# Kernel tuning notes

Hardware: AMD Instinct MI355X
Metric: run time of the kernel (lower is better)

## Reference

```python
import jax, jax.numpy as jnp
import numpy as np

N_NODES = 50000
N_EDGES = 800000
F_IN, H1, H2, N_CLASSES = 128, 200, 100, 40


def setup_inputs() -> dict:
    key = jax.random.key(0)
    ks = jax.random.split(key, 8)
    x = jax.random.normal(ks[0], (N_NODES, F_IN), dtype=jnp.float32)
    edge_index = jax.random.randint(ks[1], (2, N_EDGES), 0, N_NODES, dtype=jnp.int64)
    # Glorot-ish scaled params
    W1 = jax.random.normal(ks[2], (F_IN, H1), dtype=jnp.float32) * (1.0 / np.sqrt(F_IN))
    b1 = jnp.zeros((H1,), dtype=jnp.float32)
    W2 = jax.random.normal(ks[3], (H1, H2), dtype=jnp.float32) * (1.0 / np.sqrt(H1))
    b2 = jnp.zeros((H2,), dtype=jnp.float32)
    Wout = jax.random.normal(ks[4], (H2, N_CLASSES), dtype=jnp.float32) * (1.0 / np.sqrt(H2))
    bout = jnp.zeros((N_CLASSES,), dtype=jnp.float32)
    return {"x": x, "edge_index": edge_index, "W1": W1, "b1": b1,
            "W2": W2, "b2": b2, "Wout": Wout, "bout": bout}


def _gcn_norm(edge_index, n_nodes):
    # Add self-loops, then symmetric normalization deg^{-1/2}[src]*deg^{-1/2}[dst]
    loop = jnp.arange(n_nodes, dtype=edge_index.dtype)
    src = jnp.concatenate([edge_index[0], loop])
    dst = jnp.concatenate([edge_index[1], loop])
    deg = jax.ops.segment_sum(jnp.ones_like(dst, dtype=jnp.float32), dst,
                              num_segments=n_nodes)
    dinv = jax.lax.rsqrt(deg)  # deg >= 1 due to self-loops
    norm = dinv[src] * dinv[dst]  # [E+N]
    return src, dst, norm


def _gcn_conv(h, W, b, src, dst, norm, n_nodes):
    hw = h @ W                                   # [N, out] dense transform first
    msg = norm[:, None] * hw[src]                # [E+N, out] gather + scale
    agg = jax.ops.segment_sum(msg, dst, num_segments=n_nodes)  # scatter-add
    return agg + b


def reference(x, edge_index, W1, b1, W2, b2, Wout, bout):
    n = x.shape[0]
    src, dst, norm = _gcn_norm(edge_index, n)
    h = jax.nn.relu(_gcn_conv(x, W1, b1, src, dst, norm, n))
    # dropout is identity in eval mode
    h = jax.nn.relu(_gcn_conv(h, W2, b2, src, dst, norm, n))
    return h @ Wout + bout
```

## Files before the change

### kernel.cpp

```cpp
#include <hip/hip_runtime.h>


#define NN 50000
#define NE 800000
#define NPART 8
#define PCAP 20
#define DST 40

typedef short v8s __attribute__((ext_vector_type(8)));
typedef float f4 __attribute__((ext_vector_type(4)));
typedef ushort u8v __attribute__((ext_vector_type(8)));

static __device__ __forceinline__ ushort bf16rne(float f) {
    unsigned u = __float_as_uint(f);
    return (ushort)((u + 0x7FFFu + ((u >> 16) & 1u)) >> 16);
}
static __device__ __forceinline__ float bf16tof(ushort h) {
    return __uint_as_float(((unsigned)h) << 16);
}

#define PK1 (14 * 4 * 512)
#define PK2 (7 * 7 * 512)
#define PK3 (3 * 4 * 512)
#define ZERO_BLKS ((NN * NPART / 4 + 255) / 256)
#define PACK_BLKS ((PK1 + PK2 + PK3 + 255) / 256)

__global__ __launch_bounds__(256)
void prep_kernel(const float* __restrict__ W1, const float* __restrict__ W2,
                 const float* __restrict__ W3,
                 ushort* __restrict__ b1p, ushort* __restrict__ b2p,
                 ushort* __restrict__ b3p,
                 int* __restrict__ flag, int* __restrict__ cnt8,
                 const unsigned int* __restrict__ eiw) {
    int b = blockIdx.x;
    if (b < ZERO_BLKS) {
        int i = b * 256 + threadIdx.x;
        if (i < NN * NPART / 4) ((int4*)cnt8)[i] = make_int4(0, 0, 0, 0);
        return;
    }
    b -= ZERO_BLKS;
    if (b < PACK_BLKS) {
        int idx = b * 256 + threadIdx.x;
        const float* W; ushort* o; int q, KS, K, N;
        if (idx < PK1)                  { W = W1; o = b1p; q = idx;             KS = 4; K = 128; N = 200; }
        else if (idx < PK1 + PK2)       { W = W2; o = b2p; q = idx - PK1;       KS = 7; K = 200; N = 100; }
        else if (idx < PK1 + PK2 + PK3) { W = W3; o = b3p; q = idx - PK1 - PK2; KS = 4; K = 100; N = 40;  }
        else return;
        int tile = q / (KS * 512);
        int rem  = q % (KS * 512);
        int s    = rem / 512;
        int z    = rem % 512;
        int lane = z / 8, j = z % 8;
        int col = tile * 16 + (lane & 15);
        int k   = s * 32 + (lane >> 4) * 8 + j;
        o[q] = bf16rne((k < K && col < N) ? W[k * N + col] : 0.f);
        return;
    }
    if (threadIdx.x == 0) {
        int is64 = 1;
        for (int i = 0; i < 32; ++i)
            if (eiw[2 * i + 1] != 0u) { is64 = 0; break; }
        *flag = is64;
    }
}

__global__ __launch_bounds__(256)
void place8_kernel(const void* __restrict__ ei, const int* __restrict__ flag,
                   int* __restrict__ cnt8, ushort* __restrict__ slab) {
    int e = blockIdx.x * 256 + threadIdx.x;
    if (e >= NE) return;
    int p = blockIdx.x & 7;
    int s, d;
    if (*flag) {
        s = (int)((const long long*)ei)[e];
        d = (int)((const long long*)ei)[NE + e];
    } else {
        s = ((const int*)ei)[e];
        d = ((const int*)ei)[NE + e];
    }
    int pos = atomicAdd(&cnt8[p * NN + d], 1);
    if (pos < PCAP) slab[((size_t)p * NN + d) * PCAP + pos] = (ushort)s;
}

__global__ __launch_bounds__(256)
void build_kernel(const int* __restrict__ cnt8, const ushort* __restrict__ slab,
                  const float* __restrict__ x, ushort* __restrict__ csrF,
                  int* __restrict__ degC, float* __restrict__ dinv,
                  ushort* __restrict__ xb) {
    __shared__ float sdinv[256];
    const int t = threadIdx.x;
    const int d = blockIdx.x * 256 + t;
    if (d < NN) {
        int tot = 0, k = 0;
        ushort* __restrict__ dst = csrF + (size_t)d * DST;
        #pragma unroll
        for (int p = 0; p < NPART; ++p) {
            int c = cnt8[p * NN + d];
            tot += c;
            c = min(c, PCAP);
            const ushort* sp = slab + ((size_t)p * NN + d) * PCAP;
            for (int j = 0; j < c; ++j) {
                if (k < DST) dst[k++] = sp[j];
            }
        }
        degC[d] = k;
        float di = rsqrtf((float)(tot + 1));
        dinv[d] = di;
        sdinv[t] = di;
    }
    __syncthreads();
    const size_t base = (size_t)blockIdx.x * 256;
    #pragma unroll
    for (int it = 0; it < 16; ++it) {
        int v = it * 256 + t;
        int lrow = v >> 4;
        if (base + lrow >= NN) break;
        float di = sdinv[lrow];
        size_t g = (base + lrow) * 128 + (size_t)(v & 15) * 8;
        float4 v0 = *(const float4*)(x + g);
        float4 v1 = *(const float4*)(x + g + 4);
        *(ushort4*)(xb + g) = make_ushort4(bf16rne(di * v0.x), bf16rne(di * v0.y),
                                           bf16rne(di * v0.z), bf16rne(di * v0.w));
        *(ushort4*)(xb + g + 4) = make_ushort4(bf16rne(di * v1.x), bf16rne(di * v1.y),
                                               bf16rne(di * v1.z), bf16rne(di * v1.w));
    }
}

template <int F, int SST, int KPAD, bool BR>
__global__ __launch_bounds__(256)
void agg_kernel(const ushort* __restrict__ src, const float* __restrict__ dinv,
                const int* __restrict__ degC, const ushort* __restrict__ csrF,
                const float* __restrict__ bias, ushort* __restrict__ outp) {
    const int w = threadIdx.x >> 6, l = threadIdx.x & 63;
    const int grp = l >> 4, cp = l & 15;
    const int row = blockIdx.x * 16 + w * 4 + grp;
    const int cb = cp * 8;
    const int len = degC[row];
    const int s0 = row * DST;
    const float di = dinv[row];
    int lmax = len;
    lmax = max(lmax, __shfl_xor(lmax, 16));
    lmax = max(lmax, __shfl_xor(lmax, 32));

    float acc[8];
    u8v sv = *(const u8v*)(src + (size_t)row * SST + cb);
    #pragma unroll
    for (int q = 0; q < 8; ++q) acc[q] = bf16tof(sv[q]);

    for (int er = 0; er < lmax; er += 8) {
        int c[8];
        float m[8];
        #pragma unroll
        for (int i = 0; i < 8; ++i) {
            bool ok = (er + i) < len;
            c[i] = csrF[ok ? (s0 + er + i) : 0];
            m[i] = ok ? 1.f : 0.f;
        }
        u8v r[8];
        #pragma unroll
        for (int i = 0; i < 8; ++i)
            r[i] = *(const u8v*)(src + (size_t)c[i] * SST + cb);
        #pragma unroll
        for (int i = 0; i < 8; ++i)
            #pragma unroll
            for (int q = 0; q < 8; ++q)
                acc[q] = fmaf(bf16tof(r[i][q]), m[i], acc[q]);
    }

    u8v ov;
    #pragma unroll
    for (int q = 0; q < 8; ++q) {
        int col = cb + q;
        float v = di * acc[q];
        if constexpr (BR) v = (col < F) ? fmaxf(v + bias[col], 0.f) : 0.f;
        else              v = (col < F) ? v : 0.f;
        ov[q] = bf16rne(v);
    }
    *(u8v*)(outp + (size_t)row * KPAD + cb) = ov;
}

template <int NT, int KS, int MODE>
__global__ __launch_bounds__(256)
void mfma_gemm(const ushort* __restrict__ A, const ushort* __restrict__ B,
               float* __restrict__ Cf, ushort* __restrict__ Cb,
               const float* __restrict__ bias, const float* __restrict__ dinv,
               int M, int N, int NPAD) {
    constexpr int KP = KS * 32;
    const int tid = threadIdx.x, w = tid >> 6, l = tid & 63;
    const int arow = blockIdx.x * 64 + w * 16 + (l & 15);
    const int kg = l >> 4;
    const bool aok = arow < M;
    f4 acc[NT];
    #pragma unroll
    for (int t = 0; t < NT; ++t) acc[t] = (f4)0.f;
    const v8s zz = (v8s)0;
    const ushort* pa = A + (size_t)arow * KP + kg * 8;

    for (int s = 0; s < KS; ++s) {
        v8s a = aok ? *(const v8s*)(pa + s * 32) : zz;
        #pragma unroll
        for (int t = 0; t < NT; ++t) {
            v8s b = *(const v8s*)(B + ((size_t)(t * KS + s) * 64 + l) * 8);
            acc[t] = __builtin_amdgcn_mfma_f32_16x16x32_bf16(a, b, acc[t], 0, 0, 0);
        }
    }
    const int crow0 = blockIdx.x * 64 + w * 16 + (l >> 4) * 4;
    #pragma unroll
    for (int t = 0; t < NT; ++t) {
        int col = t * 16 + (l & 15);
        #pragma unroll
        for (int r = 0; r < 4; ++r) {
            int row = crow0 + r;
            if (row >= M) continue;
            float v = acc[t][r];
            if constexpr (MODE == 0) {
                if (col < N) Cf[(size_t)row * N + col] = v + bias[col];
            } else if constexpr (MODE == 1) {
                float o = (col < N) ? fmaxf(v + bias[col], 0.f) : 0.f;
                Cb[(size_t)row * NPAD + col] = bf16rne(o);
            } else {
                float o = (col < N) ? dinv[row] * v : 0.f;
                Cb[(size_t)row * NPAD + col] = bf16rne(o);
            }
        }
    }
}

extern "C" void kernel_launch(void* const* d_in, const int* in_sizes, int n_in,
                              void* d_out, int out_size, void* d_ws, size_t ws_size,
                              hipStream_t stream) {
    const float* x    = (const float*)d_in[0];
    const void*  ei   = d_in[1];
    const float* W1   = (const float*)d_in[2];
    const float* b1   = (const float*)d_in[3];
    const float* W2   = (const float*)d_in[4];
    const float* b2   = (const float*)d_in[5];
    const float* Wout = (const float*)d_in[6];
    const float* bout = (const float*)d_in[7];
    float* out = (float*)d_out;

    char* ws = (char*)d_ws;
    size_t off = 0;
    auto alloc = [&](size_t bytes) -> void* {
        off = (off + 255) & ~(size_t)255;
        void* p = ws + off;
        off += bytes;
        return p;
    };
    int*    flag = (int*)alloc(4);
    int*    cnt8 = (int*)alloc((size_t)NN * NPART * 4);
    int*    degC = (int*)alloc((size_t)NN * 4);
    float*  dinv = (float*)alloc((size_t)NN * 4);
    ushort* slab = (ushort*)alloc((size_t)NN * NPART * PCAP * 2);
    ushort* csrF = (ushort*)alloc((size_t)NN * DST * 2);
    ushort* xb   = (ushort*)alloc((size_t)NN * 128 * 2);
    ushort* tbuf = (ushort*)alloc((size_t)NN * 128 * 2);
    ushort* h1   = (ushort*)alloc((size_t)NN * 224 * 2);
    ushort* u    = (ushort*)alloc((size_t)NN * 128 * 2);
    ushort* h2   = (ushort*)alloc((size_t)NN * 128 * 2);
    ushort* b1p  = (ushort*)alloc((size_t)PK1 * 2);
    ushort* b2p  = (ushort*)alloc((size_t)PK2 * 2);
    ushort* b3p  = (ushort*)alloc((size_t)PK3 * 2);
    (void)ws_size; (void)in_sizes; (void)n_in; (void)out_size;

    const int PREP_BLKS = ZERO_BLKS + PACK_BLKS + 1;

    prep_kernel<<<PREP_BLKS, 256, 0, stream>>>(W1, W2, Wout, b1p, b2p, b3p,
                                               flag, cnt8, (const unsigned int*)ei);
    place8_kernel<<<(NE + 255) / 256, 256, 0, stream>>>(ei, flag, cnt8, slab);
    build_kernel<<<(NN + 255) / 256, 256, 0, stream>>>(cnt8, slab, x, csrF,
                                                       degC, dinv, xb);

    const int GA = NN / 16;
    const int GG = (NN + 63) / 64;

    agg_kernel<128, 128, 128, false><<<GA, 256, 0, stream>>>(
        xb, dinv, degC, csrF, nullptr, tbuf);
    mfma_gemm<14, 4, 1><<<GG, 256, 0, stream>>>(
        tbuf, b1p, nullptr, h1, b1, nullptr, NN, 200, 224);
    mfma_gemm<7, 7, 2><<<GG, 256, 0, stream>>>(
        h1, b2p, nullptr, u, nullptr, dinv, NN, 100, 128);
    agg_kernel<100, 128, 128, true><<<GA, 256, 0, stream>>>(
        u, dinv, degC, csrF, b2, h2);
    mfma_gemm<3, 4, 0><<<GG, 256, 0, stream>>>(
        h2, b3p, out, nullptr, bout, nullptr, NN, 40, 0);
}
```

Baseline: 191.7 us.

## Fuse layer-1 and layer-2 GEMMs via LDS, fuse final GEMM into aggregation

Merges the two dense transforms (128->200 and 200->100) into one kernel that keeps the 200-wide hidden activations in LDS instead of writing and reading them from global memory. It also fuses the output projection (100->40) into the second aggregation kernel, which runs the small MFMA on the 16 aggregated rows held in LDS. This cuts two kernel launches and removes the global round trips for h1 and h2. The cost is more LDS use and fewer concurrent blocks in the fused GEMM, and a partially idle final MFMA stage where one of the four waves does nothing.

Measured after the change: 165.5 us. -13.7%, faster.

```diff
diff --git a/kernel.cpp b/kernel.cpp
--- a/kernel.cpp
+++ b/kernel.cpp
@@ -126,11 +126,10 @@
     }
 }
 
-template <int F, int SST, int KPAD, bool BR>
-__global__ __launch_bounds__(256)
-void agg_kernel(const ushort* __restrict__ src, const float* __restrict__ dinv,
-                const int* __restrict__ degC, const ushort* __restrict__ csrF,
-                const float* __restrict__ bias, ushort* __restrict__ outp) {
+__global__ __launch_bounds__(256)
+void agg1_kernel(const ushort* __restrict__ src, const float* __restrict__ dinv,
+                 const int* __restrict__ degC, const ushort* __restrict__ csrF,
+                 ushort* __restrict__ outp) {
     const int w = threadIdx.x >> 6, l = threadIdx.x & 63;
     const int grp = l >> 4, cp = l & 15;
     const int row = blockIdx.x * 16 + w * 4 + grp;
@@ -143,7 +142,7 @@
     lmax = max(lmax, __shfl_xor(lmax, 32));
 
     float acc[8];
-    u8v sv = *(const u8v*)(src + (size_t)row * SST + cb);
+    u8v sv = *(const u8v*)(src + (size_t)row * 128 + cb);
     #pragma unroll
     for (int q = 0; q < 8; ++q) acc[q] = bf16tof(sv[q]);
 
@@ -159,7 +158,7 @@
         u8v r[8];
         #pragma unroll
         for (int i = 0; i < 8; ++i)
-            r[i] = *(const u8v*)(src + (size_t)c[i] * SST + cb);
+            r[i] = *(const u8v*)(src + (size_t)c[i] * 128 + cb);
         #pragma unroll
         for (int i = 0; i < 8; ++i)
             #pragma unroll
@@ -169,59 +168,141 @@
 
     u8v ov;
     #pragma unroll
+    for (int q = 0; q < 8; ++q) ov[q] = bf16rne(di * acc[q]);
+    *(u8v*)(outp + (size_t)row * 128 + cb) = ov;
+}
+
+__global__ __launch_bounds__(256)
+void gemm12_kernel(const ushort* __restrict__ A, const ushort* __restrict__ B1,
+                   const ushort* __restrict__ B2, const float* __restrict__ b1,
+                   const float* __restrict__ dinv, ushort* __restrict__ u) {
+    constexpr int LST = 232;
+    __shared__ ushort lh1[64 * LST];
+    const int tid = threadIdx.x, w = tid >> 6, l = tid & 63;
+    const int kg = l >> 4;
+    const int arow = blockIdx.x * 64 + w * 16 + (l & 15);
+    const bool aok = arow < NN;
+    const v8s zz = (v8s)0;
+
+    f4 o1[14];
+    #pragma unroll
+    for (int t = 0; t < 14; ++t) o1[t] = (f4)0.f;
+    const ushort* pa = A + (size_t)arow * 128 + kg * 8;
+    for (int s = 0; s < 4; ++s) {
+        v8s a = aok ? *(const v8s*)(pa + s * 32) : zz;
+        #pragma unroll
+        for (int t = 0; t < 14; ++t) {
+            v8s b = *(const v8s*)(B1 + ((size_t)(t * 4 + s) * 64 + l) * 8);
+            o1[t] = __builtin_amdgcn_mfma_f32_16x16x32_bf16(a, b, o1[t], 0, 0, 0);
+        }
+    }
+    const int lrow0 = w * 16 + ((l >> 4) << 2);
+    #pragma unroll
+    for (int t = 0; t < 14; ++t) {
+        int col = t * 16 + (l & 15);
+        float bc = (col < 200) ? b1[col] : 0.f;
+        #pragma unroll
+        for (int r = 0; r < 4; ++r) {
+            float v = (col < 200) ? fmaxf(o1[t][r] + bc, 0.f) : 0.f;
+            lh1[(lrow0 + r) * LST + col] = bf16rne(v);
+        }
+    }
+    __syncthreads();
+    f4 o2[7];
+    #pragma unroll
+    for (int t = 0; t < 7; ++t) o2[t] = (f4)0.f;
+    const int lrowA = w * 16 + (l & 15);
+    for (int s = 0; s < 7; ++s) {
+        v8s a = *(const v8s*)(&lh1[lrowA * LST + kg * 8 + s * 32]);
+        #pragma unroll
+        for (int t = 0; t < 7; ++t) {
+            v8s b = *(const v8s*)(B2 + ((size_t)(t * 7 + s) * 64 + l) * 8);
+            o2[t] = __builtin_amdgcn_mfma_f32_16x16x32_bf16(a, b, o2[t], 0, 0, 0);
+        }
+    }
+    const int crow0 = blockIdx.x * 64 + w * 16 + ((l >> 4) << 2);
+    #pragma unroll
+    for (int t = 0; t < 7; ++t) {
+        int col = t * 16 + (l & 15);
+        #pragma unroll
+        for (int r = 0; r < 4; ++r) {
+            int row = crow0 + r;
+            if (row >= NN) continue;
+            float o = (col < 100) ? dinv[row] * o2[t][r] : 0.f;
+            u[(size_t)row * 128 + col] = bf16rne(o);
+        }
+    }
+}
+
+__global__ __launch_bounds__(256)
+void agg2g3_kernel(const ushort* __restrict__ u, const float* __restrict__ dinv,
+                   const int* __restrict__ degC, const ushort* __restrict__ csrF,
+                   const ushort* __restrict__ B3, const float* __restrict__ b2,
+                   const float* __restrict__ bout, float* __restrict__ out) {
+    constexpr int LST = 136;
+    __shared__ ushort lh2[16 * LST];
+    const int w = threadIdx.x >> 6, l = threadIdx.x & 63;
+    const int grp = l >> 4, cp = l & 15;
+    const int row = blockIdx.x * 16 + w * 4 + grp;
+    const int cb = cp * 8;
+    const int len = degC[row];
+    const int s0 = row * DST;
+    const float di = dinv[row];
+    int lmax = len;
+    lmax = max(lmax, __shfl_xor(lmax, 16));
+    lmax = max(lmax, __shfl_xor(lmax, 32));
+
+    float acc[8];
+    u8v sv = *(const u8v*)(u + (size_t)row * 128 + cb);
+    #pragma unroll
+    for (int q = 0; q < 8; ++q) acc[q] = bf16tof(sv[q]);
+
+    for (int er = 0; er < lmax; er += 8) {
+        int c[8];
+        float m[8];
+        #pragma unroll
+        for (int i = 0; i < 8; ++i) {
+            bool ok = (er + i) < len;
+            c[i] = csrF[ok ? (s0 + er + i) : 0];
+            m[i] = ok ? 1.f : 0.f;
+        }
+        u8v r[8];
+        #pragma unroll
+        for (int i = 0; i < 8; ++i)
+            r[i] = *(const u8v*)(u + (size_t)c[i] * 128 + cb);
+        #pragma unroll
+        for (int i = 0; i < 8; ++i)
+            #pragma unroll
+            for (int q = 0; q < 8; ++q)
+                acc[q] = fmaf(bf16tof(r[i][q]), m[i], acc[q]);
+    }
+    u8v ov;
+    #pragma unroll
     for (int q = 0; q < 8; ++q) {
         int col = cb + q;
         float v = di * acc[q];
-        if constexpr (BR) v = (col < F) ? fmaxf(v + bias[col], 0.f) : 0.f;
-        else              v = (col < F) ? v : 0.f;
+        v = (col < 100) ? fmaxf(v + b2[col], 0.f) : 0.f;
         ov[q] = bf16rne(v);
     }
-    *(u8v*)(outp + (size_t)row * KPAD + cb) = ov;
-}
-
-template <int NT, int KS, int MODE>
-__global__ __launch_bounds__(256)
-void mfma_gemm(const ushort* __restrict__ A, const ushort* __restrict__ B,
-               float* __restrict__ Cf, ushort* __restrict__ Cb,
-               const float* __restrict__ bias, const float* __restrict__ dinv,
-               int M, int N, int NPAD) {
-    constexpr int KP = KS * 32;
-    const int tid = threadIdx.x, w = tid >> 6, l = tid & 63;
-    const int arow = blockIdx.x * 64 + w * 16 + (l & 15);
-    const int kg = l >> 4;
-    const bool aok = arow < M;
-    f4 acc[NT];
-    #pragma unroll
-    for (int t = 0; t < NT; ++t) acc[t] = (f4)0.f;
-    const v8s zz = (v8s)0;
-    const ushort* pa = A + (size_t)arow * KP + kg * 8;
-
-    for (int s = 0; s < KS; ++s) {
-        v8s a = aok ? *(const v8s*)(pa + s * 32) : zz;
-        #pragma unroll
-        for (int t = 0; t < NT; ++t) {
-            v8s b = *(const v8s*)(B + ((size_t)(t * KS + s) * 64 + l) * 8);
-            acc[t] = __builtin_amdgcn_mfma_f32_16x16x32_bf16(a, b, acc[t], 0, 0, 0);
-        }
-    }
-    const int crow0 = blockIdx.x * 64 + w * 16 + (l >> 4) * 4;
-    #pragma unroll
-    for (int t = 0; t < NT; ++t) {
-        int col = t * 16 + (l & 15);
-        #pragma unroll
-        for (int r = 0; r < 4; ++r) {
-            int row = crow0 + r;
-            if (row >= M) continue;
-            float v = acc[t][r];
-            if constexpr (MODE == 0) {
-                if (col < N) Cf[(size_t)row * N + col] = v + bias[col];
-            } else if constexpr (MODE == 1) {
-                float o = (col < N) ? fmaxf(v + bias[col], 0.f) : 0.f;
-                Cb[(size_t)row * NPAD + col] = bf16rne(o);
-            } else {
-                float o = (col < N) ? dinv[row] * v : 0.f;
-                Cb[(size_t)row * NPAD + col] = bf16rne(o);
-            }
+    const int lrow = w * 4 + grp;
+    *(u8v*)(&lh2[lrow * LST + cb]) = ov;
+    __syncthreads();
+    if (w < 3) {
+        f4 o3 = (f4)0.f;
+        const int lrowA = l & 15;
+        const int kg = l >> 4;
+        for (int s = 0; s < 4; ++s) {
+            v8s a = *(const v8s*)(&lh2[lrowA * LST + kg * 8 + s * 32]);
+            v8s b = *(const v8s*)(B3 + ((size_t)(w * 4 + s) * 64 + l) * 8);
+            o3 = __builtin_amdgcn_mfma_f32_16x16x32_bf16(a, b, o3, 0, 0, 0);
+        }
+        int col = w * 16 + (l & 15);
+        if (col < 40) {
+            const int crow0 = blockIdx.x * 16 + ((l >> 4) << 2);
+            float bo = bout[col];
+            #pragma unroll
+            for (int r = 0; r < 4; ++r)
+                out[(size_t)(crow0 + r) * 40 + col] = o3[r] + bo;
         }
     }
 }
@@ -255,9 +336,7 @@
     ushort* csrF = (ushort*)alloc((size_t)NN * DST * 2);
     ushort* xb   = (ushort*)alloc((size_t)NN * 128 * 2);
     ushort* tbuf = (ushort*)alloc((size_t)NN * 128 * 2);
-    ushort* h1   = (ushort*)alloc((size_t)NN * 224 * 2);
     ushort* u    = (ushort*)alloc((size_t)NN * 128 * 2);
-    ushort* h2   = (ushort*)alloc((size_t)NN * 128 * 2);
     ushort* b1p  = (ushort*)alloc((size_t)PK1 * 2);
     ushort* b2p  = (ushort*)alloc((size_t)PK2 * 2);
     ushort* b3p  = (ushort*)alloc((size_t)PK3 * 2);
@@ -274,14 +353,7 @@
     const int GA = NN / 16;
     const int GG = (NN + 63) / 64;
 
-    agg_kernel<128, 128, 128, false><<<GA, 256, 0, stream>>>(
-        xb, dinv, degC, csrF, nullptr, tbuf);
-    mfma_gemm<14, 4, 1><<<GG, 256, 0, stream>>>(
-        tbuf, b1p, nullptr, h1, b1, nullptr, NN, 200, 224);
-    mfma_gemm<7, 7, 2><<<GG, 256, 0, stream>>>(
-        h1, b2p, nullptr, u, nullptr, dinv, NN, 100, 128);
-    agg_kernel<100, 128, 128, true><<<GA, 256, 0, stream>>>(
-        u, dinv, degC, csrF, b2, h2);
-    mfma_gemm<3, 4, 0><<<GG, 256, 0, stream>>>(
-        h2, b3p, out, nullptr, bout, nullptr, NN, 40, 0);
-}
+    agg1_kernel<<<GA, 256, 0, stream>>>(xb, dinv, degC, csrF, tbuf);
+    gemm12_kernel<<<GG, 256, 0, stream>>>(tbuf, b1p, b2p, b1, dinv, u);
+    agg2g3_kernel<<<GA, 256, 0, stream>>>(u, dinv, degC, csrF, b3p, b2, bout, out);
+}
```
